# Kernel tuning notes

Hardware: AMD Instinct MI355X
Metric: run time of the kernel (lower is better)

## Reference

```python
import jax, jax.numpy as jnp
import numpy as np
from jax import lax


def setup_inputs() -> dict:
    key = jax.random.key(0)
    k0, k1, k2, k3 = jax.random.split(key, 4)
    B, C, H, W = 16, 64, 192, 192
    K = 3
    x0 = jax.random.normal(k0, (B, C, H, W), dtype=jnp.float32)
    d = jax.random.normal(k1, (B, C), dtype=jnp.float32)
    w1 = jax.random.normal(k2, (C, C), dtype=jnp.float32) * 0.05
    w2 = jax.random.normal(k3, (C * K * K, C), dtype=jnp.float32) * 0.05
    return {"x0": x0, "d": d, "w1": w1, "w2": w2}


def reference(x0, d, w1, w2):
    b, c, h, w = x0.shape
    k = int(round((w2.shape[0] // c) ** 0.5))  # kernel_size
    # kernel-generating MLP: Linear(C,C,bias=False) -> LeakyReLU(0.1) -> Linear(C,C*k*k,bias=False)
    hid = jax.nn.leaky_relu(d @ w1.T, negative_slope=0.1)          # (B, C)
    ker = (hid @ w2.T).reshape(b * c, 1, k, k)                      # (B*C, 1, k, k)
    pad = (k - 1) // 2
    # per-(batch,channel) dynamic depthwise conv: groups = B*C
    out = lax.conv_general_dilated(
        x0.reshape(1, b * c, h, w),
        ker,
        window_strides=(1, 1),
        padding=[(pad, pad), (pad, pad)],
        dimension_numbers=("NCHW", "OIHW", "NCHW"),
        feature_group_count=b * c,
    )
    return out.reshape(b, c, h, w)
```

## Files before the change

### kernel.cpp

```cpp
#include <hip/hip_runtime.h>


#define BB 16
#define CC 64
#define HH 192
#define WW 192
#define KERLEN (CC * 9)
#define QW (WW / 4)
#define RPT 4
#define TPP (QW * (HH / RPT))
#define BPP (TPP / 256)

typedef float f4 __attribute__((ext_vector_type(4)));

__global__ __launch_bounds__(256) void gen_kernels(
    const float* __restrict__ d,
    const float* __restrict__ w1,
    const float* __restrict__ w2,
    float* __restrict__ ker)
{
    __shared__ float dd[CC];
    __shared__ float hid[CC];
    const int b = blockIdx.x;
    const int t = threadIdx.x;

    if (t < CC) dd[t] = d[b * CC + t];
    __syncthreads();

    if (t < CC) {
        const float* w1r = w1 + t * CC;
        float acc = 0.f;
        #pragma unroll 8
        for (int m = 0; m < CC; ++m) acc += dd[m] * w1r[m];
        hid[t] = acc > 0.f ? acc : 0.1f * acc;
    }
    __syncthreads();

    for (int o = t; o < KERLEN; o += 256) {
        const float* w2r = w2 + o * CC;
        float acc = 0.f;
        #pragma unroll 8
        for (int k = 0; k < CC; ++k) acc += hid[k] * w2r[k];
        ker[b * KERLEN + o] = acc;
    }
}

__global__ __launch_bounds__(256, 8) void dconv3x3_v10(
    const float* __restrict__ x,
    const float* __restrict__ ker,
    float* __restrict__ out)
{
    const int blk = blockIdx.x;
    const int bc  = blk / BPP;
    const int sub = blk - bc * BPP;

    const float* kp = ker + bc * 9;
    const float k00 = kp[0], k01 = kp[1], k02 = kp[2];
    const float k10 = kp[3], k11 = kp[4], k12 = kp[5];
    const float k20 = kp[6], k21 = kp[7], k22 = kp[8];

    const int task = sub * 256 + threadIdx.x;
    const int rg   = task / QW;
    const int qw   = task - rg * QW;
    const int w    = qw * 4;
    const int r0   = rg * RPT;

    const bool hasL = (qw > 0);
    const bool hasR = (qw < QW - 1);
    const int  offL = hasL ? -1 : 0;
    const int  offR = hasR ?  4 : 0;

    const float* __restrict__ xp = x   + (size_t)bc * HH * WW + w;
    float* __restrict__       op = out + (size_t)bc * HH * WW + w;

    f4    c[RPT + 2];
    float l[RPT + 2], r[RPT + 2];
    const f4 zero = {0.f, 0.f, 0.f, 0.f};

    #pragma unroll
    for (int j = 0; j < RPT + 2; ++j) {
        const int rr  = r0 - 1 + j;
        const int rcl = rr < 0 ? 0 : (rr >= HH ? HH - 1 : rr);
        const float* p = xp + rcl * WW;
        const f4 v     = __builtin_nontemporal_load((const f4*)p);
        const float lv = __builtin_nontemporal_load(p + offL);
        const float rv = __builtin_nontemporal_load(p + offR);
        const bool ok  = (rr >= 0) & (rr < HH);
        c[j] = ok ? v : zero;
        l[j] = (ok && hasL) ? lv : 0.f;
        r[j] = (ok && hasR) ? rv : 0.f;
    }

    #pragma unroll
    for (int i = 0; i < RPT; ++i) {
        const f4 ca = c[i], cb = c[i + 1], cd = c[i + 2];
        const float la = l[i], lb = l[i + 1], lc = l[i + 2];
        const float ra = r[i], rb = r[i + 1], rc = r[i + 2];

        f4 o;
        o.x = k00 * la   + k01 * ca.x + k02 * ca.y
            + k10 * lb   + k11 * cb.x + k12 * cb.y
            + k20 * lc   + k21 * cd.x + k22 * cd.y;
        o.y = k00 * ca.x + k01 * ca.y + k02 * ca.z
            + k10 * cb.x + k11 * cb.y + k12 * cb.z
            + k20 * cd.x + k21 * cd.y + k22 * cd.z;
        o.z = k00 * ca.y + k01 * ca.z + k02 * ca.w
            + k10 * cb.y + k11 * cb.z + k12 * cb.w
            + k20 * cd.y + k21 * cd.z + k22 * cd.w;
        o.w = k00 * ca.z + k01 * ca.w + k02 * ra
            + k10 * cb.z + k11 * cb.w + k12 * rb
            + k20 * cd.z + k21 * cd.w + k22 * rc;

        *(f4*)(op + (size_t)(r0 + i) * WW) = o;
    }
}

extern "C" void kernel_launch(void* const* d_in, const int* in_sizes, int n_in,
                              void* d_out, int out_size, void* d_ws, size_t ws_size,
                              hipStream_t stream) {
    const float* x0 = (const float*)d_in[0];
    const float* d  = (const float*)d_in[1];
    const float* w1 = (const float*)d_in[2];
    const float* w2 = (const float*)d_in[3];
    float* out = (float*)d_out;
    float* ker = (float*)d_ws;

    gen_kernels<<<BB, 256, 0, stream>>>(d, w1, w2, ker);
    dconv3x3_v10<<<BB * CC * BPP, 256, 0, stream>>>(x0, ker, out);
}
```

Before: 293.6 us.

## Switch depthwise conv to grid-stride persistent blocks with two rows per task

```diff
diff --git a/kernel.cpp b/kernel.cpp
--- a/kernel.cpp
+++ b/kernel.cpp
@@ -7,9 +7,13 @@
 #define WW 192
 #define KERLEN (CC * 9)
 #define QW (WW / 4)
-#define RPT 4
-#define TPP (QW * (HH / RPT))
-#define BPP (TPP / 256)
+#define NPLANE (BB * CC)
+#define PPP (96 * QW)
+#define TOTALP (NPLANE * PPP)
+#define NBLK 2048
+#define NTHR (NBLK * 256)
+#define NIT (TOTALP / NTHR)
+#define PLSZ (HH * WW)
 
 typedef float f4 __attribute__((ext_vector_type(4)));
 
@@ -41,77 +45,93 @@
         float acc = 0.f;
         #pragma unroll 8
         for (int k = 0; k < CC; ++k) acc += hid[k] * w2r[k];
-        ker[b * KERLEN + o] = acc;
+        const int c = o / 9;
+        const int j = o - c * 9;
+        ker[(b * CC + c) * 16 + j] = acc;
     }
 }
 
-__global__ __launch_bounds__(256, 8) void dconv3x3_v10(
+__global__ __launch_bounds__(256) void dconv3x3_v11(
     const float* __restrict__ x,
     const float* __restrict__ ker,
     float* __restrict__ out)
 {
-    const int blk = blockIdx.x;
-    const int bc  = blk / BPP;
-    const int sub = blk - bc * BPP;
-
-    const float* kp = ker + bc * 9;
-    const float k00 = kp[0], k01 = kp[1], k02 = kp[2];
-    const float k10 = kp[3], k11 = kp[4], k12 = kp[5];
-    const float k20 = kp[6], k21 = kp[7], k22 = kp[8];
-
-    const int task = sub * 256 + threadIdx.x;
-    const int rg   = task / QW;
-    const int qw   = task - rg * QW;
-    const int w    = qw * 4;
-    const int r0   = rg * RPT;
-
-    const bool hasL = (qw > 0);
-    const bool hasR = (qw < QW - 1);
-    const int  offL = hasL ? -1 : 0;
-    const int  offR = hasR ?  4 : 0;
-
-    const float* __restrict__ xp = x   + (size_t)bc * HH * WW + w;
-    float* __restrict__       op = out + (size_t)bc * HH * WW + w;
-
-    f4    c[RPT + 2];
-    float l[RPT + 2], r[RPT + 2];
+    const int tid = blockIdx.x * 256 + threadIdx.x;
     const f4 zero = {0.f, 0.f, 0.f, 0.f};
 
-    #pragma unroll
-    for (int j = 0; j < RPT + 2; ++j) {
-        const int rr  = r0 - 1 + j;
-        const int rcl = rr < 0 ? 0 : (rr >= HH ? HH - 1 : rr);
-        const float* p = xp + rcl * WW;
-        const f4 v     = __builtin_nontemporal_load((const f4*)p);
-        const float lv = __builtin_nontemporal_load(p + offL);
-        const float rv = __builtin_nontemporal_load(p + offR);
-        const bool ok  = (rr >= 0) & (rr < HH);
-        c[j] = ok ? v : zero;
-        l[j] = (ok && hasL) ? lv : 0.f;
-        r[j] = (ok && hasR) ? rv : 0.f;
-    }
+    #pragma unroll 3
+    for (int it = 0; it < NIT; ++it) {
+        const int idx = tid + it * NTHR;
+        const int p   = idx / PPP;
+        const int rem = idx - p * PPP;
+        const int rp  = rem / QW;
+        const int q   = rem - rp * QW;
 
-    #pragma unroll
-    for (int i = 0; i < RPT; ++i) {
-        const f4 ca = c[i], cb = c[i + 1], cd = c[i + 2];
-        const float la = l[i], lb = l[i + 1], lc = l[i + 2];
-        const float ra = r[i], rb = r[i + 1], rc = r[i + 2];
+        const int r0 = rp * 2;
+        const bool okm = (rp > 0);
+        const bool okp = (rp < 95);
+        const bool hasL = (q > 0);
+        const bool hasR = (q < QW - 1);
+        const int offL = hasL ? -1 : 0;
+        const int offR = hasR ?  4 : 0;
 
-        f4 o;
-        o.x = k00 * la   + k01 * ca.x + k02 * ca.y
-            + k10 * lb   + k11 * cb.x + k12 * cb.y
-            + k20 * lc   + k21 * cd.x + k22 * cd.y;
-        o.y = k00 * ca.x + k01 * ca.y + k02 * ca.z
-            + k10 * cb.x + k11 * cb.y + k12 * cb.z
-            + k20 * cd.x + k21 * cd.y + k22 * cd.z;
-        o.z = k00 * ca.y + k01 * ca.z + k02 * ca.w
-            + k10 * cb.y + k11 * cb.z + k12 * cb.w
-            + k20 * cd.y + k21 * cd.z + k22 * cd.w;
-        o.w = k00 * ca.z + k01 * ca.w + k02 * ra
-            + k10 * cb.z + k11 * cb.w + k12 * rb
-            + k20 * cd.z + k21 * cd.w + k22 * rc;
+        const float* kp = ker + p * 16;
+        const f4 ka = *(const f4*)kp;
+        const f4 kb = *(const f4*)(kp + 4);
+        const float k22 = kp[8];
+        const float k00 = ka.x, k01 = ka.y, k02 = ka.z, k10 = ka.w;
+        const float k11 = kb.x, k12 = kb.y, k20 = kb.z, k21 = kb.w;
 
-        *(f4*)(op + (size_t)(r0 + i) * WW) = o;
+        const float* base = x + (size_t)p * PLSZ + r0 * WW + q * 4;
+
+        const float* pa = base + (okm ? -WW : 0);
+        const float* pb = base;
+        const float* pc = base + WW;
+        const float* pd = base + (okp ? 2 * WW : WW);
+
+        f4 va = *(const f4*)pa;  float lA = pa[offL], rA = pa[offR];
+        f4 vb = *(const f4*)pb;  float lB = pb[offL], rB = pb[offR];
+        f4 vc = *(const f4*)pc;  float lC = pc[offL], rC = pc[offR];
+        f4 vd = *(const f4*)pd;  float lD = pd[offL], rD = pd[offR];
+
+        va = okm ? va : zero;
+        lA = (okm && hasL) ? lA : 0.f;  rA = (okm && hasR) ? rA : 0.f;
+        vd = okp ? vd : zero;
+        lD = (okp && hasL) ? lD : 0.f;  rD = (okp && hasR) ? rD : 0.f;
+        lB = hasL ? lB : 0.f;  rB = hasR ? rB : 0.f;
+        lC = hasL ? lC : 0.f;  rC = hasR ? rC : 0.f;
+
+        f4 o0;
+        o0.x = k00 * lA   + k01 * va.x + k02 * va.y
+             + k10 * lB   + k11 * vb.x + k12 * vb.y
+             + k20 * lC   + k21 * vc.x + k22 * vc.y;
+        o0.y = k00 * va.x + k01 * va.y + k02 * va.z
+             + k10 * vb.x + k11 * vb.y + k12 * vb.z
+             + k20 * vc.x + k21 * vc.y + k22 * vc.z;
+        o0.z = k00 * va.y + k01 * va.z + k02 * va.w
+             + k10 * vb.y + k11 * vb.z + k12 * vb.w
+             + k20 * vc.y + k21 * vc.z + k22 * vc.w;
+        o0.w = k00 * va.z + k01 * va.w + k02 * rA
+             + k10 * vb.z + k11 * vb.w + k12 * rB
+             + k20 * vc.z + k21 * vc.w + k22 * rC;
+
+        f4 o1;
+        o1.x = k00 * lB   + k01 * vb.x + k02 * vb.y
+             + k10 * lC   + k11 * vc.x + k12 * vc.y
+             + k20 * lD   + k21 * vd.x + k22 * vd.y;
+        o1.y = k00 * vb.x + k01 * vb.y + k02 * vb.z
+             + k10 * vc.x + k11 * vc.y + k12 * vc.z
+             + k20 * vd.x + k21 * vd.y + k22 * vd.z;
+        o1.z = k00 * vb.y + k01 * vb.z + k02 * vb.w
+             + k10 * vc.y + k11 * vc.z + k12 * vc.w
+             + k20 * vd.y + k21 * vd.z + k22 * vd.w;
+        o1.w = k00 * vb.z + k01 * vb.w + k02 * rB
+             + k10 * vc.z + k11 * vc.w + k12 * rC
+             + k20 * vd.z + k21 * vd.w + k22 * rD;
+
+        float* op = out + (size_t)p * PLSZ + r0 * WW + q * 4;
+        *(f4*)op        = o0;
+        *(f4*)(op + WW) = o1;
     }
 }
 
@@ -126,5 +146,5 @@
     float* ker = (float*)d_ws;
 
     gen_kernels<<<BB, 256, 0, stream>>>(d, w1, w2, ker);
-    dconv3x3_v10<<<BB * CC * BPP, 256, 0, stream>>>(x0, ker, out);
+    dconv3x3_v11<<<NBLK, 256, 0, stream>>>(x0, ker, out);
 }
```

Result: no change. 290.5 us (-1.1%).

## Widen per-thread column tile and share halo columns via wavefront shuffles

Applied to the files above, without the earlier changes.

```diff
diff --git a/kernel.cpp b/kernel.cpp
--- a/kernel.cpp
+++ b/kernel.cpp
@@ -6,9 +6,11 @@
 #define HH 192
 #define WW 192
 #define KERLEN (CC * 9)
-#define QW (WW / 4)
+#define PLSZ (HH * WW)
 #define RPT 4
-#define TPP (QW * (HH / RPT))
+#define NLANE 16
+#define COLS 12
+#define TPP (NLANE * (HH / RPT))
 #define BPP (TPP / 256)
 
 typedef float f4 __attribute__((ext_vector_type(4)));
@@ -41,77 +43,90 @@
         float acc = 0.f;
         #pragma unroll 8
         for (int k = 0; k < CC; ++k) acc += hid[k] * w2r[k];
-        ker[b * KERLEN + o] = acc;
+        const int c = o / 9;
+        const int j = o - c * 9;
+        ker[(b * CC + c) * 16 + j] = acc;
     }
 }
 
-__global__ __launch_bounds__(256, 8) void dconv3x3_v10(
+__global__ __launch_bounds__(256) void dconv3x3_v12(
     const float* __restrict__ x,
     const float* __restrict__ ker,
     float* __restrict__ out)
 {
-    const int blk = blockIdx.x;
-    const int bc  = blk / BPP;
-    const int sub = blk - bc * BPP;
+    const int blk  = blockIdx.x;
+    const int p    = blk / BPP;
+    const int chnk = blk - p * BPP;
+    const int task = chnk * 256 + threadIdx.x;
+    const int rg   = task >> 4;
+    const int m    = task & 15;
+    const int r0   = rg * RPT;
+    const int col  = m * COLS;
 
-    const float* kp = ker + bc * 9;
+    const float* kp = ker + p * 16;
     const float k00 = kp[0], k01 = kp[1], k02 = kp[2];
     const float k10 = kp[3], k11 = kp[4], k12 = kp[5];
     const float k20 = kp[6], k21 = kp[7], k22 = kp[8];
 
-    const int task = sub * 256 + threadIdx.x;
-    const int rg   = task / QW;
-    const int qw   = task - rg * QW;
-    const int w    = qw * 4;
-    const int r0   = rg * RPT;
+    const float* __restrict__ xp = x   + (size_t)p * PLSZ + col;
+    float* __restrict__       op = out + (size_t)p * PLSZ + col;
 
-    const bool hasL = (qw > 0);
-    const bool hasR = (qw < QW - 1);
-    const int  offL = hasL ? -1 : 0;
-    const int  offR = hasR ?  4 : 0;
-
-    const float* __restrict__ xp = x   + (size_t)bc * HH * WW + w;
-    float* __restrict__       op = out + (size_t)bc * HH * WW + w;
-
-    f4    c[RPT + 2];
-    float l[RPT + 2], r[RPT + 2];
+    const bool hasL = (m > 0);
+    const bool hasR = (m < NLANE - 1);
     const f4 zero = {0.f, 0.f, 0.f, 0.f};
 
+    f4 c[RPT + 2][3];
     #pragma unroll
     for (int j = 0; j < RPT + 2; ++j) {
         const int rr  = r0 - 1 + j;
         const int rcl = rr < 0 ? 0 : (rr >= HH ? HH - 1 : rr);
-        const float* p = xp + rcl * WW;
-        const f4 v     = __builtin_nontemporal_load((const f4*)p);
-        const float lv = __builtin_nontemporal_load(p + offL);
-        const float rv = __builtin_nontemporal_load(p + offR);
-        const bool ok  = (rr >= 0) & (rr < HH);
-        c[j] = ok ? v : zero;
-        l[j] = (ok && hasL) ? lv : 0.f;
-        r[j] = (ok && hasR) ? rv : 0.f;
+        const f4* pr  = (const f4*)(xp + rcl * WW);
+        c[j][0] = pr[0];
+        c[j][1] = pr[1];
+        c[j][2] = pr[2];
     }
+
+    float le[RPT + 2], re[RPT + 2];
+    #pragma unroll
+    for (int j = 0; j < RPT + 2; ++j) {
+        const int rr = r0 - 1 + j;
+        const bool ok = (unsigned)rr < (unsigned)HH;
+        c[j][0] = ok ? c[j][0] : zero;
+        c[j][1] = ok ? c[j][1] : zero;
+        c[j][2] = ok ? c[j][2] : zero;
+        const float lv = __shfl_up(c[j][2].w, 1);
+        const float rv = __shfl_down(c[j][0].x, 1);
+        le[j] = hasL ? lv : 0.f;
+        re[j] = hasR ? rv : 0.f;
+    }
+
+    auto part = [&](int j, int s, float kl, float kc, float kr) -> f4 {
+        const f4 cc     = c[j][s];
+        const float lft = (s == 0) ? le[j] : c[j][s - 1].w;
+        const float rgt = (s == 2) ? re[j] : c[j][s + 1].x;
+        f4 t;
+        t.x = kl * lft  + kc * cc.x + kr * cc.y;
+        t.y = kl * cc.x + kc * cc.y + kr * cc.z;
+        t.z = kl * cc.y + kc * cc.z + kr * cc.w;
+        t.w = kl * cc.z + kc * cc.w + kr * rgt;
+        return t;
+    };
 
     #pragma unroll
     for (int i = 0; i < RPT; ++i) {
-        const f4 ca = c[i], cb = c[i + 1], cd = c[i + 2];
-        const float la = l[i], lb = l[i + 1], lc = l[i + 2];
-        const float ra = r[i], rb = r[i + 1], rc = r[i + 2];
-
-        f4 o;
-        o.x = k00 * la   + k01 * ca.x + k02 * ca.y
-            + k10 * lb   + k11 * cb.x + k12 * cb.y
-            + k20 * lc   + k21 * cd.x + k22 * cd.y;
-        o.y = k00 * ca.x + k01 * ca.y + k02 * ca.z
-            + k10 * cb.x + k11 * cb.y + k12 * cb.z
-            + k20 * cd.x + k21 * cd.y + k22 * cd.z;
-        o.z = k00 * ca.y + k01 * ca.z + k02 * ca.w
-            + k10 * cb.y + k11 * cb.z + k12 * cb.w
-            + k20 * cd.y + k21 * cd.z + k22 * cd.w;
-        o.w = k00 * ca.z + k01 * ca.w + k02 * ra
-            + k10 * cb.z + k11 * cb.w + k12 * rb
-            + k20 * cd.z + k21 * cd.w + k22 * rc;
-
-        *(f4*)(op + (size_t)(r0 + i) * WW) = o;
+        f4* orow = (f4*)(op + (size_t)(r0 + i) * WW);
+        #pragma unroll
+        for (int s = 0; s < 3; ++s) {
+            const f4 t0 = part(i,     s, k00, k01, k02);
+            const f4 t1 = part(i + 1, s, k10, k11, k12);
+            const f4 t2 = part(i + 2, s, k20, k21, k22);
+            f4 o;
+            o.x = t0.x + t1.x + t2.x;
+            o.y = t0.y + t1.y + t2.y;
+            o.z = t0.z + t1.z + t2.z;
+            o.w = t0.w + t1.w + t2.w;
+            orow[s] = o;
+        }
     }
 }
 
@@ -126,5 +141,5 @@
     float* ker = (float*)d_ws;
 
     gen_kernels<<<BB, 256, 0, stream>>>(d, w1, w2, ker);
-    dconv3x3_v10<<<BB * CC * BPP, 256, 0, stream>>>(x0, ker, out);
+    dconv3x3_v12<<<BB * CC * BPP, 256, 0, stream>>>(x0, ker, out);
 }
```

After: 275.5 us. 1.07x faster.
